# Performance work log

Measured on AMD Instinct MI355X. Metric: run time of the kernel, lower is better.

## Reference

```python
import jax, jax.numpy as jnp
import numpy as np

B, M, C_SEED, NSAMPLE = 2, 1024, 512, 16
BASE_RADIUS, HMIN, HMAX = 0.05, -0.02, 0.04
RADII = [BASE_RADIUS * s for s in (0.25, 0.5, 0.75, 1.0)]
EPS = 1e-5


def _bn_relu(x, g, be, m, v):
    # eval-mode BatchNorm2d over channel axis 1, then ReLU
    s = jax.lax.rsqrt(v + EPS) * g
    return jax.nn.relu((x - m[None, :, None, None]) * s[None, :, None, None] + be[None, :, None, None])


def _crop(xyz, feats, rot, local, radius, params):
    # xyz: (B,N,3); feats: (B,C,N); rot: (B,M,3,3); local: (B,M,N,3) point coords in each seed's rotated frame
    W1, b1, g1, be1, m1, v1, W2, b2, g2, be2, m2, v2 = params
    d2 = local[..., 1] ** 2 + local[..., 2] ** 2
    mask = (d2 < radius * radius) & (local[..., 0] > HMIN) & (local[..., 0] < HMAX)
    # cylinder_query semantics: take first NSAMPLE in-cylinder indices (index order), pad with first found
    order = jnp.argsort(jnp.where(mask, 0, 1).astype(jnp.int32), axis=-1)  # stable sort: valid first
    idx = order[..., :NSAMPLE]                                   # (B,M,ns)
    valid = jnp.take_along_axis(mask, idx, axis=-1)
    idx = jnp.where(valid, idx, idx[..., :1])                    # seed itself is always in-cylinder
    g_xyz = jax.vmap(lambda p, i: p[i])(xyz, idx)                # (B,M,ns,3)
    g_xyz = (g_xyz - xyz[:, :, None, :]) / radius                # center + normalize_xyz
    g_xyz = jnp.einsum('bmnd,bmde->bmne', g_xyz, rot)            # rotate_xyz
    g_feat = jax.vmap(lambda f, i: f[:, i])(feats, idx)          # (B,C,M,ns)
    x = jnp.concatenate([g_xyz.transpose(0, 3, 1, 2), g_feat], axis=1)  # (B,3+C,M,ns)
    x = _bn_relu(jnp.einsum('bcmn,oc->bomn', x, W1) + b1[None, :, None, None], g1, be1, m1, v1)
    x = _bn_relu(jnp.einsum('bcmn,oc->bomn', x, W2) + b2[None, :, None, None], g2, be2, m2, v2)
    return jnp.max(x, axis=-1)                                   # (B,256,M) max-pool over neighbors


def setup_inputs() -> dict:
    key = jax.random.key(0)
    ks = jax.random.split(key, 12)
    C1 = 3 + C_SEED
    inp = {
        'seed_xyz': jax.random.uniform(ks[0], (B, M, 3), dtype=jnp.float32),
        'seed_features': jax.random.normal(ks[1], (B, C_SEED, M), dtype=jnp.float32),
        'vp_rot': jax.random.normal(ks[2], (B, M, 3, 3), dtype=jnp.float32),
        'crop_W1': jax.random.normal(ks[3], (4, 256, C1), dtype=jnp.float32) * 0.05,
        'crop_b1': jax.random.normal(ks[4], (4, 256), dtype=jnp.float32) * 0.05,
        'crop_g1': jnp.ones((4, 256), jnp.float32),
        'crop_be1': jnp.zeros((4, 256), jnp.float32),
        'crop_m1': jnp.zeros((4, 256), jnp.float32),
        'crop_v1': jnp.ones((4, 256), jnp.float32),
        'crop_W2': jax.random.normal(ks[5], (4, 256, 256), dtype=jnp.float32) * 0.05,
        'crop_b2': jax.random.normal(ks[6], (4, 256), dtype=jnp.float32) * 0.05,
        'crop_g2': jnp.ones((4, 256), jnp.float32),
        'crop_be2': jnp.zeros((4, 256), jnp.float32),
        'crop_m2': jnp.zeros((4, 256), jnp.float32),
        'crop_v2': jnp.ones((4, 256), jnp.float32),
        'fuse_W': jax.random.normal(ks[7], (256, 1024), dtype=jnp.float32) * 0.05,
        'fuse_b': jax.random.normal(ks[8], (256,), dtype=jnp.float32) * 0.05,
        'gate_W': jax.random.normal(ks[9], (256, 256), dtype=jnp.float32) * 0.05,
        'gate_b': jax.random.normal(ks[10], (256,), dtype=jnp.float32) * 0.05,
        'trans_W': jax.random.normal(ks[11], (256, C_SEED), dtype=jnp.float32) * 0.05,
        'trans_b': jnp.zeros((256,), jnp.float32),
    }
    return inp


def reference(seed_xyz, seed_features, vp_rot, crop_W1, crop_b1, crop_g1, crop_be1, crop_m1, crop_v1,
              crop_W2, crop_b2, crop_g2, crop_be2, crop_m2, crop_v2,
              fuse_W, fuse_b, gate_W, gate_b, trans_W, trans_b):
    # local[b,m,n] = rot[b,m]^T @ (xyz[b,n] - xyz[b,m])  (row-major rot -> diff @ rot)
    diff = seed_xyz[:, None, :, :] - seed_xyz[:, :, None, :]        # (B,M,N,3)
    local = jnp.einsum('bmnd,bmde->bmne', diff, vp_rot)
    outs = []
    for s, radius in enumerate(RADII):
        params = (crop_W1[s], crop_b1[s], crop_g1[s], crop_be1[s], crop_m1[s], crop_v1[s],
                  crop_W2[s], crop_b2[s], crop_g2[s], crop_be2[s], crop_m2[s], crop_v2[s])
        outs.append(_crop(seed_xyz, seed_features, vp_rot, local, radius, params))
    cat = jnp.concatenate(outs, axis=1)                              # (B,1024,M)
    fused = jnp.einsum('bcm,oc->bom', cat, fuse_W) + fuse_b[None, :, None]
    seed_t = jnp.einsum('bcm,oc->bom', seed_features, trans_W) + trans_b[None, :, None]
    gate = jax.nn.sigmoid(jnp.einsum('bcm,oc->bom', seed_t, gate_W) + gate_b[None, :, None])
    return fused + gate * seed_t                                     # (B,256,M)
```

## Files before the change

### kernel.cpp

```cpp
#include <hip/hip_runtime.h>
#include <math.h>

typedef __attribute__((ext_vector_type(8))) short short8;
typedef __attribute__((ext_vector_type(4))) float f32x4;

__device__ __forceinline__ unsigned short bf16_bits(float f) {
  unsigned u = __float_as_uint(f);
  u += 0x7fffu + ((u >> 16) & 1u);
  return (unsigned short)(u >> 16);
}

__global__ __launch_bounds__(256) void k0b_prep(
    const float* __restrict__ W1, const float* __restrict__ b1, const float* __restrict__ g1,
    const float* __restrict__ be1, const float* __restrict__ m1, const float* __restrict__ v1,
    const float* __restrict__ W2, const float* __restrict__ b2, const float* __restrict__ g2,
    const float* __restrict__ be2, const float* __restrict__ m2, const float* __restrict__ v2,
    unsigned short* __restrict__ W2f, float4* __restrict__ xyzb,
    float* __restrict__ bias2c, float* __restrict__ s1arr) {
  const int so = blockIdx.x;
  const int j  = threadIdx.x;
  const int s = so >> 8, o = so & 255;
  const float s2 = rsqrtf(v2[so] + 1e-5f) * g2[so];
  const int t = o >> 4, r = o & 15;
  const int ks = j >> 5, hi = (j >> 3) & 3, i = j & 7;
  const int l = hi * 16 + r;
  W2f[(size_t)s * 65536 + (size_t)((ks * 16 + t) << 9) + l * 8 + i] =
      bf16_bits(W2[(size_t)so * 256 + j] * s2);
  if (j == 0) {
    const float s1 = rsqrtf(v1[so] + 1e-5f) * g1[so];
    const float* wr = W1 + (size_t)so * 515;
    xyzb[so] = make_float4(wr[0] * s1, wr[1] * s1, wr[2] * s1,
                           (b1[so] - m1[so]) * s1 + be1[so]);
    bias2c[so] = (b2[so] - m2[so]) * s2 + be2[so];
    s1arr[so] = s1;
  }
}

__global__ __launch_bounds__(256) void k0_neighbors(
    const float* __restrict__ xyz, const float* __restrict__ rot,
    int* __restrict__ idx_arr, float4* __restrict__ gxyz4) {
  const int wid = threadIdx.x >> 6, lane = threadIdx.x & 63;
  const int gw = blockIdx.x * 4 + wid;
  const int b = gw >> 10, m = gw & 1023;
  const float* pm = xyz + (size_t)(b * 1024 + m) * 3;
  const float cx = pm[0], cy = pm[1], cz = pm[2];
  const float* pr = rot + (size_t)(b * 1024 + m) * 9;
  float R[9];
#pragma unroll
  for (int i = 0; i < 9; ++i) R[i] = pr[i];
  const float radf[4] = {0.0125f, 0.025f, 0.0375f, 0.05f};
  const float rad2[4] = {(float)(0.0125 * 0.0125), (float)(0.025 * 0.025),
                         (float)(0.0375 * 0.0375), (float)(0.05 * 0.05)};
  int cnt[4] = {0, 0, 0, 0};
  int firstn[4] = {0, 0, 0, 0};
  float f0x[4] = {0, 0, 0, 0}, f0y[4] = {0, 0, 0, 0}, f0z[4] = {0, 0, 0, 0};
  for (int n0 = 0; n0 < 1024; n0 += 64) {
    const int n = n0 + lane;
    const float* pn = xyz + (size_t)(b * 1024 + n) * 3;
    const float dx = pn[0] - cx, dy = pn[1] - cy, dz = pn[2] - cz;
    const float l0 = dx * R[0] + dy * R[3] + dz * R[6];
    const float l1 = dx * R[1] + dy * R[4] + dz * R[7];
    const float l2 = dx * R[2] + dy * R[5] + dz * R[8];
    const float d2 = l1 * l1 + l2 * l2;
    const bool hok = (l0 > -0.02f) && (l0 < 0.04f);
#pragma unroll
    for (int s = 0; s < 4; ++s) {
      if (cnt[s] >= 16) continue;
      const bool p = hok && (d2 < rad2[s]);
      const unsigned long long bal = __ballot(p);
      if (bal == 0ull) continue;
      if (cnt[s] == 0) {
        const int src = __builtin_ctzll(bal);
        firstn[s] = n0 + src;
        f0x[s] = __shfl(l0, src);
        f0y[s] = __shfl(l1, src);
        f0z[s] = __shfl(l2, src);
      }
      const int rank = __popcll(bal & ((1ull << lane) - 1ull));
      const int slot = cnt[s] + rank;
      if (p && slot < 16) {
        const size_t base = ((size_t)((s * 2 + b) * 1024 + m)) * 16 + slot;
        idx_arr[base] = n;
        gxyz4[base] = make_float4(l0 / radf[s], l1 / radf[s], l2 / radf[s], 0.f);
      }
      cnt[s] = min(cnt[s] + (int)__popcll(bal), 16);
    }
  }
#pragma unroll
  for (int s = 0; s < 4; ++s) {
    if (lane < 16 && lane >= cnt[s]) {
      const size_t base = ((size_t)((s * 2 + b) * 1024 + m)) * 16 + lane;
      idx_arr[base] = firstn[s];
      gxyz4[base] = make_float4(f0x[s] / radf[s], f0y[s] / radf[s], f0z[s] / radf[s], 0.f);
    }
  }
}

__global__ __launch_bounds__(256) void k1_f1(
    const float* __restrict__ feats, const float* __restrict__ W1,
    const float* __restrict__ s1arr, float* __restrict__ F1) {
  __shared__ float At[16][68];
  __shared__ float Bt[16][68];
  const int bid = blockIdx.x;
  const int ogt = bid & 15, nt = (bid >> 4) & 15, b = bid >> 8;
  const int og0 = ogt * 64, n0 = nt * 64;
  const int tx = threadIdx.x & 15, ty = threadIdx.x >> 4;
  float acc[4][4] = {};
  for (int c0 = 0; c0 < 512; c0 += 16) {
#pragma unroll
    for (int it = 0; it < 4; ++it) {
      const int t = threadIdx.x + it * 256;
      { const int cc = t >> 6, nn = t & 63;
        At[cc][nn] = feats[((size_t)(b * 512 + c0 + cc)) * 1024 + n0 + nn]; }
      { const int cc = t & 15, nn = t >> 4;
        const int og = og0 + nn;
        Bt[cc][nn] = W1[(size_t)og * 515 + 3 + c0 + cc] * s1arr[og]; }
    }
    __syncthreads();
#pragma unroll
    for (int cc = 0; cc < 16; ++cc) {
      const float4 a = *(const float4*)&At[cc][ty * 4];
      const float4 bv = *(const float4*)&Bt[cc][tx * 4];
      const float av[4] = {a.x, a.y, a.z, a.w};
      const float bw[4] = {bv.x, bv.y, bv.z, bv.w};
#pragma unroll
      for (int i = 0; i < 4; ++i)
#pragma unroll
        for (int j = 0; j < 4; ++j) acc[i][j] = fmaf(av[i], bw[j], acc[i][j]);
    }
    __syncthreads();
  }
  const int s = og0 >> 8;
  const int obase = (og0 & 255) + tx * 4;
#pragma unroll
  for (int i = 0; i < 4; ++i) {
    const int n = n0 + ty * 4 + i;
    float4 w;
    w.x = acc[i][0]; w.y = acc[i][1]; w.z = acc[i][2]; w.w = acc[i][3];
    *(float4*)&F1[(((size_t)(s * 2 + b)) * 1024 + n) * 256 + obase] = w;
  }
}

__global__ __launch_bounds__(256) void k2_layer2(
    const int* __restrict__ idx_arr, const float4* __restrict__ gxyz4,
    const float* __restrict__ F1, const unsigned short* __restrict__ W2f,
    const float4* __restrict__ xyzb, const float* __restrict__ bias2c,
    float* __restrict__ cat) {
  const int wid = threadIdx.x >> 6, lane = threadIdx.x & 63;
  const int bid = blockIdx.x;
  const int mg = bid & 255, b = (bid >> 8) & 1, s = bid >> 9;
  const int m = mg * 4 + wid;
  const int r = lane & 15, hi = lane >> 4;
  const size_t sb = (size_t)((s * 2 + b) * 1024 + m) * 16 + r;
  const int n = idx_arr[sb];
  const float4 g = gxyz4[sb];
  const float* __restrict__ f1row = F1 + ((size_t)((s * 2 + b) * 1024) + n) * 256;
  const unsigned short* __restrict__ w2f = W2f + (size_t)s * 65536;
  const float4* __restrict__ xbs = xyzb + s * 256;

  float4 pf[16];
#pragma unroll
  for (int ks = 0; ks < 8; ++ks) {
    const int j0 = ks * 32 + hi * 8;
    pf[ks * 2]     = *(const float4*)(f1row + j0);
    pf[ks * 2 + 1] = *(const float4*)(f1row + j0 + 4);
  }

  f32x4 acc[16];
#pragma unroll
  for (int t = 0; t < 16; ++t) { acc[t][0] = 0.f; acc[t][1] = 0.f; acc[t][2] = 0.f; acc[t][3] = 0.f; }

#pragma unroll
  for (int ks = 0; ks < 8; ++ks) {
    const unsigned short* wk = w2f + ((size_t)(ks * 16) << 9) + lane * 8;
    short8 bf[16];
#pragma unroll
    for (int t = 0; t < 16; ++t)
      bf[t] = *(const short8*)(wk + ((size_t)t << 9));
    const int j0 = ks * 32 + hi * 8;
    const float4 fa = pf[ks * 2], fb = pf[ks * 2 + 1];
    const float fv[8] = {fa.x, fa.y, fa.z, fa.w, fb.x, fb.y, fb.z, fb.w};
    short8 af;
#pragma unroll
    for (int i = 0; i < 8; ++i) {
      const float4 xb = xbs[j0 + i];
      float v = fv[i] + xb.w;
      v = fmaf(g.x, xb.x, v);
      v = fmaf(g.y, xb.y, v);
      v = fmaf(g.z, xb.z, v);
      v = fmaxf(v, 0.f);
      af[i] = (short)bf16_bits(v);
    }
#pragma unroll
    for (int t = 0; t < 16; ++t)
      acc[t] = __builtin_amdgcn_mfma_f32_16x16x32_bf16(af, bf[t], acc[t], 0, 0, 0);
  }

  float* __restrict__ catrow = cat + ((size_t)(b * 1024 + m)) * 1024 + s * 256;
#pragma unroll
  for (int t = 0; t < 16; ++t) {
    const float bc = bias2c[s * 256 + t * 16 + r];
    float mv = fmaxf(acc[t][0] + bc, 0.f);
    mv = fmaxf(mv, fmaxf(acc[t][1] + bc, 0.f));
    mv = fmaxf(mv, fmaxf(acc[t][2] + bc, 0.f));
    mv = fmaxf(mv, fmaxf(acc[t][3] + bc, 0.f));
    mv = fmaxf(mv, __shfl_xor(mv, 16));
    mv = fmaxf(mv, __shfl_xor(mv, 32));
    if (hi == 0) catrow[t * 16 + r] = mv;
  }
}


__global__ __launch_bounds__(256) void k3_trans(
    const float* __restrict__ feats, const float* __restrict__ W,
    const float* __restrict__ bias, float* __restrict__ outp) {
  __shared__ float At[16][68];
  __shared__ float Bt[16][36];
  const int bid = blockIdx.x;
  const int ot = bid & 7, nt = (bid >> 3) & 15, b = bid >> 7;
  const int og0 = ot * 32, m0 = nt * 64;
  const int tx = threadIdx.x & 7, ty = threadIdx.x >> 3;
  float acc[2][4] = {};
  for (int c0 = 0; c0 < 512; c0 += 16) {
#pragma unroll
    for (int it = 0; it < 4; ++it) {
      const int t = threadIdx.x + it * 256;
      const int cc = t >> 6, nn = t & 63;
      At[cc][nn] = feats[((size_t)(b * 512 + c0 + cc)) * 1024 + m0 + nn];
    }
#pragma unroll
    for (int it = 0; it < 2; ++it) {
      const int t = threadIdx.x + it * 256;
      const int cc = t & 15, nn = t >> 4;
      Bt[cc][nn] = W[(size_t)(og0 + nn) * 512 + c0 + cc];
    }
    __syncthreads();
#pragma unroll
    for (int cc = 0; cc < 16; ++cc) {
      const float2 a = *(const float2*)&At[cc][ty * 2];
      const float4 bv = *(const float4*)&Bt[cc][tx * 4];
      const float av[2] = {a.x, a.y};
      const float bw[4] = {bv.x, bv.y, bv.z, bv.w};
#pragma unroll
      for (int i = 0; i < 2; ++i)
#pragma unroll
        for (int j = 0; j < 4; ++j) acc[i][j] = fmaf(av[i], bw[j], acc[i][j]);
    }
    __syncthreads();
  }
#pragma unroll
  for (int j = 0; j < 4; ++j) {
    const int og = og0 + tx * 4 + j;
    const float bb = bias[og];
#pragma unroll
    for (int i = 0; i < 2; ++i)
      outp[((size_t)(b * 256 + og)) * 1024 + m0 + ty * 2 + i] = acc[i][j] + bb;
  }
}

__global__ __launch_bounds__(256) void k3_fuse(
    const float* __restrict__ cat, const float* __restrict__ W,
    const float* __restrict__ bias, float* __restrict__ outp) {
  __shared__ float At[16][68];
  __shared__ float Bt[16][36];
  const int bid = blockIdx.x;
  const int ot = bid & 7, nt = (bid >> 3) & 15, b = bid >> 7;
  const int og0 = ot * 32, m0 = nt * 64;
  const int tx = threadIdx.x & 7, ty = threadIdx.x >> 3;
  float acc[2][4] = {};
  for (int c0 = 0; c0 < 1024; c0 += 16) {
#pragma unroll
    for (int it = 0; it < 4; ++it) {
      const int t = threadIdx.x + it * 256;
      const int mm = t >> 4, cj = t & 15;
      At[cj][mm] = cat[((size_t)(b * 1024 + m0 + mm)) * 1024 + c0 + cj];
    }
#pragma unroll
    for (int it = 0; it < 2; ++it) {
      const int t = threadIdx.x + it * 256;
      const int cc = t & 15, nn = t >> 4;
      Bt[cc][nn] = W[(size_t)(og0 + nn) * 1024 + c0 + cc];
    }
    __syncthreads();
#pragma unroll
    for (int cc = 0; cc < 16; ++cc) {
      const float2 a = *(const float2*)&At[cc][ty * 2];
      const float4 bv = *(const float4*)&Bt[cc][tx * 4];
      const float av[2] = {a.x, a.y};
      const float bw[4] = {bv.x, bv.y, bv.z, bv.w};
#pragma unroll
      for (int i = 0; i < 2; ++i)
#pragma unroll
        for (int j = 0; j < 4; ++j) acc[i][j] = fmaf(av[i], bw[j], acc[i][j]);
    }
    __syncthreads();
  }
#pragma unroll
  for (int j = 0; j < 4; ++j) {
    const int og = og0 + tx * 4 + j;
    const float bb = bias[og];
#pragma unroll
    for (int i = 0; i < 2; ++i)
      outp[((size_t)(b * 256 + og)) * 1024 + m0 + ty * 2 + i] = acc[i][j] + bb;
  }
}

__global__ __launch_bounds__(256) void k3_gate(
    const float* __restrict__ seedt, const float* __restrict__ W,
    const float* __restrict__ bias, const float* __restrict__ fused,
    float* __restrict__ outp) {
  __shared__ float At[16][68];
  __shared__ float Bt[16][36];
  const int bid = blockIdx.x;
  const int ot = bid & 7, nt = (bid >> 3) & 15, b = bid >> 7;
  const int og0 = ot * 32, m0 = nt * 64;
  const int tx = threadIdx.x & 7, ty = threadIdx.x >> 3;
  float acc[2][4] = {};
  for (int c0 = 0; c0 < 256; c0 += 16) {
#pragma unroll
    for (int it = 0; it < 4; ++it) {
      const int t = threadIdx.x + it * 256;
      const int cc = t >> 6, nn = t & 63;
      At[cc][nn] = seedt[((size_t)(b * 256 + c0 + cc)) * 1024 + m0 + nn];
    }
#pragma unroll
    for (int it = 0; it < 2; ++it) {
      const int t = threadIdx.x + it * 256;
      const int cc = t & 15, nn = t >> 4;
      Bt[cc][nn] = W[(size_t)(og0 + nn) * 256 + c0 + cc];
    }
    __syncthreads();
#pragma unroll
    for (int cc = 0; cc < 16; ++cc) {
      const float2 a = *(const float2*)&At[cc][ty * 2];
      const float4 bv = *(const float4*)&Bt[cc][tx * 4];
      const float av[2] = {a.x, a.y};
      const float bw[4] = {bv.x, bv.y, bv.z, bv.w};
#pragma unroll
      for (int i = 0; i < 2; ++i)
#pragma unroll
        for (int j = 0; j < 4; ++j) acc[i][j] = fmaf(av[i], bw[j], acc[i][j]);
    }
    __syncthreads();
  }
#pragma unroll
  for (int j = 0; j < 4; ++j) {
    const int og = og0 + tx * 4 + j;
    const float gb = bias[og];
#pragma unroll
    for (int i = 0; i < 2; ++i) {
      const size_t oidx = ((size_t)(b * 256 + og)) * 1024 + m0 + ty * 2 + i;
      const float a = acc[i][j] + gb;
      const float gv = 1.f / (1.f + expf(-a));
      outp[oidx] = fused[oidx] + gv * seedt[oidx];
    }
  }
}

extern "C" void kernel_launch(void* const* d_in, const int* in_sizes, int n_in,
                              void* d_out, int out_size, void* d_ws, size_t ws_size,
                              hipStream_t stream) {
  (void)in_sizes; (void)n_in; (void)out_size; (void)ws_size;
  const float* seed_xyz  = (const float*)d_in[0];
  const float* seed_feat = (const float*)d_in[1];
  const float* vp_rot    = (const float*)d_in[2];
  const float* cW1  = (const float*)d_in[3];
  const float* cb1  = (const float*)d_in[4];
  const float* cg1  = (const float*)d_in[5];
  const float* cbe1 = (const float*)d_in[6];
  const float* cm1  = (const float*)d_in[7];
  const float* cv1  = (const float*)d_in[8];
  const float* cW2  = (const float*)d_in[9];
  const float* cb2  = (const float*)d_in[10];
  const float* cg2  = (const float*)d_in[11];
  const float* cbe2 = (const float*)d_in[12];
  const float* cm2  = (const float*)d_in[13];
  const float* cv2  = (const float*)d_in[14];
  const float* fuse_W  = (const float*)d_in[15];
  const float* fuse_b  = (const float*)d_in[16];
  const float* gate_W  = (const float*)d_in[17];
  const float* gate_b  = (const float*)d_in[18];
  const float* trans_W = (const float*)d_in[19];
  const float* trans_b = (const float*)d_in[20];

  char* ws = (char*)d_ws;
  float4* gxyz4        = (float4*)(ws + 0);
  float4* xyzb         = (float4*)(ws + 2097152);
  float* F1            = (float*)(ws + 2113536);
  float* cat           = (float*)(ws + 10502144);
  float* seedt         = (float*)(ws + 18890752);
  float* fusedb        = (float*)(ws + 20987904);
  int* idx_arr         = (int*)(ws + 23085056);
  unsigned short* W2f  = (unsigned short*)(ws + 23609344);
  float* bias2c        = (float*)(ws + 24133632);
  float* s1arr         = (float*)(ws + 24137728);

  hipLaunchKernelGGL(k0b_prep, dim3(1024), dim3(256), 0, stream,
                     cW1, cb1, cg1, cbe1, cm1, cv1, cW2, cb2, cg2, cbe2, cm2, cv2,
                     W2f, xyzb, bias2c, s1arr);
  hipLaunchKernelGGL(k0_neighbors, dim3(512), dim3(256), 0, stream,
                     seed_xyz, vp_rot, idx_arr, gxyz4);
  hipLaunchKernelGGL(k1_f1, dim3(512), dim3(256), 0, stream,
                     seed_feat, cW1, s1arr, F1);
  hipLaunchKernelGGL(k2_layer2, dim3(2048), dim3(256), 0, stream,
                     idx_arr, gxyz4, F1, W2f, xyzb, bias2c, cat);
  hipLaunchKernelGGL(k3_trans, dim3(256), dim3(256), 0, stream,
                     seed_feat, trans_W, trans_b, seedt);
  hipLaunchKernelGGL(k3_fuse, dim3(256), dim3(256), 0, stream,
                     cat, fuse_W, fuse_b, fusedb);
  hipLaunchKernelGGL(k3_gate, dim3(256), dim3(256), 0, stream,
                     seedt, gate_W, gate_b, fusedb, (float*)d_out);
}
```

Before: 298.5 us.

## Split neighbor search per scale with early exit; use inline-asm loads in layer2

The neighbor kernel now gives each scale its own wave, launching four times as many blocks. Each wave stops scanning once it has found 16 neighbors, where before one wave scanned all four scales serially until every one was full. The layer-2 kernel replaces compiler-generated global loads with inline-asm dwordx4 loads followed by explicit waitcnt and sched barriers, to control load issue order. This trades more redundant point loads across waves, and the risk that the explicit waits block compiler latency hiding, for more parallelism and less serial work in the neighbor search.

```diff
diff --git a/kernel.cpp b/kernel.cpp
--- a/kernel.cpp
+++ b/kernel.cpp
@@ -41,20 +41,23 @@
     int* __restrict__ idx_arr, float4* __restrict__ gxyz4) {
   const int wid = threadIdx.x >> 6, lane = threadIdx.x & 63;
   const int gw = blockIdx.x * 4 + wid;
-  const int b = gw >> 10, m = gw & 1023;
+  const int s = gw >> 11, bm = gw & 2047;
+  const int b = bm >> 10, m = bm & 1023;
   const float* pm = xyz + (size_t)(b * 1024 + m) * 3;
   const float cx = pm[0], cy = pm[1], cz = pm[2];
   const float* pr = rot + (size_t)(b * 1024 + m) * 9;
   float R[9];
 #pragma unroll
   for (int i = 0; i < 9; ++i) R[i] = pr[i];
-  const float radf[4] = {0.0125f, 0.025f, 0.0375f, 0.05f};
-  const float rad2[4] = {(float)(0.0125 * 0.0125), (float)(0.025 * 0.025),
-                         (float)(0.0375 * 0.0375), (float)(0.05 * 0.05)};
-  int cnt[4] = {0, 0, 0, 0};
-  int firstn[4] = {0, 0, 0, 0};
-  float f0x[4] = {0, 0, 0, 0}, f0y[4] = {0, 0, 0, 0}, f0z[4] = {0, 0, 0, 0};
+  const float radf_tab[4] = {0.0125f, 0.025f, 0.0375f, 0.05f};
+  const float rad2_tab[4] = {(float)(0.0125 * 0.0125), (float)(0.025 * 0.025),
+                             (float)(0.0375 * 0.0375), (float)(0.05 * 0.05)};
+  const float radf = radf_tab[s];
+  const float rad2 = rad2_tab[s];
+  int cnt = 0, firstn = 0;
+  float f0x = 0.f, f0y = 0.f, f0z = 0.f;
   for (int n0 = 0; n0 < 1024; n0 += 64) {
+    if (cnt >= 16) break;
     const int n = n0 + lane;
     const float* pn = xyz + (size_t)(b * 1024 + n) * 3;
     const float dx = pn[0] - cx, dy = pn[1] - cy, dz = pn[2] - cz;
@@ -62,37 +65,29 @@
     const float l1 = dx * R[1] + dy * R[4] + dz * R[7];
     const float l2 = dx * R[2] + dy * R[5] + dz * R[8];
     const float d2 = l1 * l1 + l2 * l2;
-    const bool hok = (l0 > -0.02f) && (l0 < 0.04f);
-#pragma unroll
-    for (int s = 0; s < 4; ++s) {
-      if (cnt[s] >= 16) continue;
-      const bool p = hok && (d2 < rad2[s]);
-      const unsigned long long bal = __ballot(p);
-      if (bal == 0ull) continue;
-      if (cnt[s] == 0) {
-        const int src = __builtin_ctzll(bal);
-        firstn[s] = n0 + src;
-        f0x[s] = __shfl(l0, src);
-        f0y[s] = __shfl(l1, src);
-        f0z[s] = __shfl(l2, src);
-      }
-      const int rank = __popcll(bal & ((1ull << lane) - 1ull));
-      const int slot = cnt[s] + rank;
-      if (p && slot < 16) {
-        const size_t base = ((size_t)((s * 2 + b) * 1024 + m)) * 16 + slot;
-        idx_arr[base] = n;
-        gxyz4[base] = make_float4(l0 / radf[s], l1 / radf[s], l2 / radf[s], 0.f);
-      }
-      cnt[s] = min(cnt[s] + (int)__popcll(bal), 16);
-    }
-  }
-#pragma unroll
-  for (int s = 0; s < 4; ++s) {
-    if (lane < 16 && lane >= cnt[s]) {
-      const size_t base = ((size_t)((s * 2 + b) * 1024 + m)) * 16 + lane;
-      idx_arr[base] = firstn[s];
-      gxyz4[base] = make_float4(f0x[s] / radf[s], f0y[s] / radf[s], f0z[s] / radf[s], 0.f);
-    }
+    const bool p = (l0 > -0.02f) && (l0 < 0.04f) && (d2 < rad2);
+    const unsigned long long bal = __ballot(p);
+    if (bal == 0ull) continue;
+    if (cnt == 0) {
+      const int src = __builtin_ctzll(bal);
+      firstn = n0 + src;
+      f0x = __shfl(l0, src);
+      f0y = __shfl(l1, src);
+      f0z = __shfl(l2, src);
+    }
+    const int rank = __popcll(bal & ((1ull << lane) - 1ull));
+    const int slot = cnt + rank;
+    if (p && slot < 16) {
+      const size_t base = ((size_t)((s * 2 + b) * 1024 + m)) * 16 + slot;
+      idx_arr[base] = n;
+      gxyz4[base] = make_float4(l0 / radf, l1 / radf, l2 / radf, 0.f);
+    }
+    cnt = min(cnt + (int)__popcll(bal), 16);
+  }
+  if (lane < 16 && lane >= cnt) {
+    const size_t base = ((size_t)((s * 2 + b) * 1024 + m)) * 16 + lane;
+    idx_arr[base] = firstn;
+    gxyz4[base] = make_float4(f0x / radf, f0y / radf, f0z / radf, 0.f);
   }
 }
 
@@ -155,16 +150,18 @@
   const int n = idx_arr[sb];
   const float4 g = gxyz4[sb];
   const float* __restrict__ f1row = F1 + ((size_t)((s * 2 + b) * 1024) + n) * 256;
-  const unsigned short* __restrict__ w2f = W2f + (size_t)s * 65536;
+  const unsigned short* __restrict__ wbase = W2f + (size_t)s * 65536 + lane * 8;
   const float4* __restrict__ xbs = xyzb + s * 256;
 
-  float4 pf[16];
+  f32x4 pf[16];
 #pragma unroll
   for (int ks = 0; ks < 8; ++ks) {
     const int j0 = ks * 32 + hi * 8;
-    pf[ks * 2]     = *(const float4*)(f1row + j0);
-    pf[ks * 2 + 1] = *(const float4*)(f1row + j0 + 4);
-  }
+    asm volatile("global_load_dwordx4 %0, %1, off" : "=&v"(pf[ks * 2])     : "v"(f1row + j0));
+    asm volatile("global_load_dwordx4 %0, %1, off" : "=&v"(pf[ks * 2 + 1]) : "v"(f1row + j0 + 4));
+  }
+  asm volatile("s_waitcnt vmcnt(0)");
+  __builtin_amdgcn_sched_barrier(0);
 
   f32x4 acc[16];
 #pragma unroll
@@ -172,14 +169,14 @@
 
 #pragma unroll
   for (int ks = 0; ks < 8; ++ks) {
-    const unsigned short* wk = w2f + ((size_t)(ks * 16) << 9) + lane * 8;
     short8 bf[16];
 #pragma unroll
     for (int t = 0; t < 16; ++t)
-      bf[t] = *(const short8*)(wk + ((size_t)t << 9));
+      asm volatile("global_load_dwordx4 %0, %1, off"
+                   : "=&v"(bf[t]) : "v"(wbase + ((size_t)(ks * 16 + t) << 9)));
     const int j0 = ks * 32 + hi * 8;
-    const float4 fa = pf[ks * 2], fb = pf[ks * 2 + 1];
-    const float fv[8] = {fa.x, fa.y, fa.z, fa.w, fb.x, fb.y, fb.z, fb.w};
+    const f32x4 fa = pf[ks * 2], fb = pf[ks * 2 + 1];
+    const float fv[8] = {fa[0], fa[1], fa[2], fa[3], fb[0], fb[1], fb[2], fb[3]};
     short8 af;
 #pragma unroll
     for (int i = 0; i < 8; ++i) {
@@ -191,6 +188,8 @@
       v = fmaxf(v, 0.f);
       af[i] = (short)bf16_bits(v);
     }
+    asm volatile("s_waitcnt vmcnt(0)");
+    __builtin_amdgcn_sched_barrier(0);
 #pragma unroll
     for (int t = 0; t < 16; ++t)
       acc[t] = __builtin_amdgcn_mfma_f32_16x16x32_bf16(af, bf[t], acc[t], 0, 0, 0);
@@ -398,7 +397,7 @@
   hipLaunchKernelGGL(k0b_prep, dim3(1024), dim3(256), 0, stream,
                      cW1, cb1, cg1, cbe1, cm1, cv1, cW2, cb2, cg2, cbe2, cm2, cv2,
                      W2f, xyzb, bias2c, s1arr);
-  hipLaunchKernelGGL(k0_neighbors, dim3(512), dim3(256), 0, stream,
+  hipLaunchKernelGGL(k0_neighbors, dim3(2048), dim3(256), 0, stream,
                      seed_xyz, vp_rot, idx_arr, gxyz4);
   hipLaunchKernelGGL(k1_f1, dim3(512), dim3(256), 0, stream,
                      seed_feat, cW1, s1arr, F1);
```

New measurement: 322.3 us. 8.0% more time.
